# Optimization experiments

Hardware: AMD Instinct MI355X
Metric: run time of the kernel (lower is better)

## Reference

```python
import jax, jax.numpy as jnp
import numpy as np
from jax.scipy.linalg import expm

B, S, D = 8, 2048, 1024          # batch, seq, input_dim
C, CD = 16, 64                   # num_concepts, concept_dim
L = C * CD                       # latent_dim = 1024
ALPHA, BETA = 0.3, 1.0
LN_EPS = 1e-5                    # torch nn.LayerNorm default


def layer_norm(x, g, b):
    m = jnp.mean(x, axis=-1, keepdims=True)
    v = jnp.mean(jnp.square(x - m), axis=-1, keepdims=True)
    return (x - m) * jax.lax.rsqrt(v + LN_EPS) * g + b


def setup_inputs() -> dict:
    key = jax.random.key(0)
    ks = jax.random.split(key, 8)
    sc = 0.02
    return {
        "x": jax.random.normal(ks[0], (B, S, D), jnp.float32),
        # encoder: Linear(D, 2L) + LayerNorm(2L)
        "enc_w": jax.random.normal(ks[1], (2 * L, D), jnp.float32) * sc,
        "enc_b": jnp.zeros((2 * L,), jnp.float32),
        "enc_g": jnp.ones((2 * L,), jnp.float32),
        "enc_bt": jnp.zeros((2 * L,), jnp.float32),
        # DAG weights [C, C] (torch inits zeros; use small random for non-trivial math)
        "dag_w": jax.random.normal(ks[2], (C, C), jnp.float32) * 0.1,
        # per-concept transforms: Linear(CD,CD) -> LN(CD) -> ReLU -> Linear(CD,CD), stacked over C
        "cw1": jax.random.normal(ks[3], (C, CD, CD), jnp.float32) * sc,
        "cb1": jnp.zeros((C, CD), jnp.float32),
        "cg": jnp.ones((C, CD), jnp.float32),
        "cbt": jnp.zeros((C, CD), jnp.float32),
        "cw2": jax.random.normal(ks[4], (C, CD, CD), jnp.float32) * sc,
        "cb2": jnp.zeros((C, CD), jnp.float32),
        # decoder: Linear(L,L) -> LN(L) -> ReLU -> Linear(L,D)
        "dec_w1": jax.random.normal(ks[5], (L, L), jnp.float32) * sc,
        "dec_b1": jnp.zeros((L,), jnp.float32),
        "dec_g": jnp.ones((L,), jnp.float32),
        "dec_bt": jnp.zeros((L,), jnp.float32),
        "dec_w2": jax.random.normal(ks[6], (D, L), jnp.float32) * sc,
        "dec_b2": jnp.zeros((D,), jnp.float32),
    }


def reference(x, enc_w, enc_b, enc_g, enc_bt, dag_w, cw1, cb1, cg, cbt, cw2, cb2,
              dec_w1, dec_b1, dec_g, dec_bt, dec_w2, dec_b2):
    # ---- encode ----
    h = layer_norm(jnp.einsum('bsd,kd->bsk', x, enc_w) + enc_b, enc_g, enc_bt)  # [B,S,2L]
    mu, logvar = jnp.split(h, 2, axis=-1)                                        # [B,S,L] each
    z = mu  # eval-mode reparameterize

    # ---- causal transform ----
    zc = z.reshape(B, S, C, CD)                                   # [B,S,C,CD]
    dag = jnp.tril(jax.nn.softplus(dag_w), k=-1)                  # [C,C]
    z_causal = zc + jnp.einsum('ij,bsjd->bsid', dag, zc)          # [B,S,C,CD]

    # per-concept Linear -> LN -> ReLU -> Linear, batched over concept axis
    t = jnp.einsum('bsce,cde->bscd', z_causal, cw1) + cb1         # [B,S,C,CD]
    t = layer_norm(t, cg, cbt)
    t = jax.nn.relu(t)
    t = jnp.einsum('bsce,cde->bscd', t, cw2) + cb2
    z_t = t.reshape(B, S, L)

    # ---- decode ----
    d = layer_norm(jnp.einsum('bsl,kl->bsk', z_t, dec_w1) + dec_b1, dec_g, dec_bt)
    d = jax.nn.relu(d)
    x_recon = jnp.einsum('bsl,dl->bsd', d, dec_w2) + dec_b2        # [B,S,D]

    # ---- losses ----
    recon_loss = jnp.mean(jnp.square(x_recon - x))
    kl_loss = -0.5 * jnp.mean(1.0 + logvar - jnp.square(mu) - jnp.exp(logvar))
    dag_loss = jnp.sum(jnp.abs(dag)) + jnp.trace(expm(dag))
    total_loss = recon_loss + ALPHA * kl_loss + BETA * dag_loss
    return x_recon, total_loss, kl_loss, recon_loss, dag_loss
```

## Files before the change

kernel.cpp:

```cpp
#include <hip/hip_runtime.h>
#include <stdint.h>


#define NTOK   16384
#define DIM    1024
#define NC     16
#define CD     64
#define NOUT_ELEMS 16777216

typedef float f32x4 __attribute__((ext_vector_type(4)));
typedef __bf16 bf16x8 __attribute__((ext_vector_type(8)));
typedef unsigned short u16x4 __attribute__((ext_vector_type(4)));
typedef unsigned short u16x8 __attribute__((ext_vector_type(8)));

__device__ float g_scal[3];
__device__ float g_part[512];

__device__ __forceinline__ float b2f(uint16_t u) {
  union { uint32_t i; float f; } v; v.i = ((uint32_t)u) << 16; return v.f;
}
__device__ __forceinline__ uint16_t f2b(float f) {
  union { float f; uint32_t i; } v; v.f = f;
  uint32_t x = v.i;
  return (uint16_t)((x + 0x7fffu + ((x >> 16) & 1u)) >> 16);
}

__device__ __forceinline__ void gload_lds16(const uint16_t* g, uint16_t* l) {
  __builtin_amdgcn_global_load_lds(
      (const __attribute__((address_space(1))) void*)g,
      (__attribute__((address_space(3))) void*)l, 16, 0, 0);
}

__device__ __forceinline__ void cvt8(const float* s, uint16_t* d) {
  const f32x4 a = *(const f32x4*)s;
  const f32x4 b = *(const f32x4*)(s + 4);
  u16x8 o;
  o[0]=f2b(a[0]); o[1]=f2b(a[1]); o[2]=f2b(a[2]); o[3]=f2b(a[3]);
  o[4]=f2b(b[0]); o[5]=f2b(b[1]); o[6]=f2b(b[2]); o[7]=f2b(b[3]);
  *(u16x8*)d = o;
}

__global__ __launch_bounds__(256) void cvt_x_kernel(
    const float* __restrict__ src, uint16_t* __restrict__ dst)
{
  const int i = blockIdx.x * 256 + threadIdx.x;
  cvt8(src + (size_t)i * 8, dst + (size_t)i * 8);
}

__global__ __launch_bounds__(256) void cvt_weights_kernel(
    const float* __restrict__ ew, const float* __restrict__ d1,
    const float* __restrict__ d2, const float* __restrict__ c1,
    const float* __restrict__ c2, uint16_t* __restrict__ out)
{
  const int i = blockIdx.x * 256 + threadIdx.x;
  const float* src; uint16_t* dst; int off;
  if (i < 262144)      { src = ew; dst = out;           off = i; }
  else if (i < 393216) { src = d1; dst = out + 2097152; off = i - 262144; }
  else if (i < 524288) { src = d2; dst = out + 3145728; off = i - 393216; }
  else if (i < 532480) { src = c1; dst = out + 4194304; off = i - 524288; }
  else                 { src = c2; dst = out + 4259840; off = i - 532480; }
  cvt8(src + (size_t)off * 8, dst + (size_t)off * 8);
}

template<int BM, int BN, int WM, int WN, typename TC, bool SPLIT, bool RECON>
__global__ __launch_bounds__(256) void gemm_bt_kernel(
    const uint16_t* __restrict__ A, const uint16_t* __restrict__ Wm,
    const float* __restrict__ bias, TC* __restrict__ C0, TC* __restrict__ C1,
    const float* __restrict__ Xref,
    int K, int lda, int ldw, int ldc)
{
  constexpr int BK = 64;
  static_assert(WM * WN == 4, "4 waves");
  constexpr int MI = BM / (WM * 16);
  constexpr int NI = BN / (WN * 16);
  constexpr int AI = (BM * BK * 2) / 4096;
  constexpr int WI = (BN * BK * 2) / 4096;

  __shared__ __align__(16) uint16_t lds[BM * BK + BN * BK];
  uint16_t* As = lds;
  uint16_t* Ws = lds + BM * BK;

  const int tid  = threadIdx.x;
  const int wave = tid >> 6;
  const int lane = tid & 63;
  const int q    = lane >> 4;
  const int r16  = lane & 15;
  const int wm   = wave / WN;
  const int wn   = wave % WN;

  const int bm = blockIdx.x * BM;
  const int bn = blockIdx.y * BN;

  const int sr = tid >> 3;
  const int pc = tid & 7;

  f32x4 acc[MI][NI] = {};

  for (int k0 = 0; k0 < K; k0 += BK) {
#pragma unroll
    for (int i = 0; i < AI; ++i) {
      const int r = i * 32 + sr;
      const int c = pc ^ (r & 7);
      const uint16_t* g = A + (size_t)(bm + r) * lda + k0 + c * 8;
      gload_lds16(g, (uint16_t*)((char*)As + i * 4096 + wave * 1024));
    }
#pragma unroll
    for (int i = 0; i < WI; ++i) {
      const int r = i * 32 + sr;
      const int c = pc ^ (r & 7);
      const uint16_t* g = Wm + (size_t)(bn + r) * ldw + k0 + c * 8;
      gload_lds16(g, (uint16_t*)((char*)Ws + i * 4096 + wave * 1024));
    }
    __syncthreads();

#pragma unroll
    for (int ks = 0; ks < 2; ++ks) {
      bf16x8 af[MI], wf[NI];
#pragma unroll
      for (int mi = 0; mi < MI; ++mi) {
        const int row = wm * (MI * 16) + mi * 16 + r16;
        const int c   = (ks * 4 + q) ^ (row & 7);
        af[mi] = *(const bf16x8*)(As + row * BK + c * 8);
      }
#pragma unroll
      for (int ni = 0; ni < NI; ++ni) {
        const int col = wn * (NI * 16) + ni * 16 + r16;
        const int c   = (ks * 4 + q) ^ (col & 7);
        wf[ni] = *(const bf16x8*)(Ws + col * BK + c * 8);
      }
#pragma unroll
      for (int mi = 0; mi < MI; ++mi)
#pragma unroll
        for (int ni = 0; ni < NI; ++ni)
          acc[mi][ni] = __builtin_amdgcn_mfma_f32_16x16x32_bf16(
              af[mi], wf[ni], acc[mi][ni], 0, 0, 0);
    }
    __syncthreads();
  }

  TC* Cq = C0;
  int cb = bn;
  if constexpr (SPLIT) {
    if (bn >= 1024) { Cq = C1; cb = bn - 1024; }
  }
  float rsum = 0.f;
#pragma unroll
  for (int ni = 0; ni < NI; ++ni) {
    const int loc = wn * (NI * 16) + ni * 16 + r16;
    const float bv = bias[bn + loc];
#pragma unroll
    for (int mi = 0; mi < MI; ++mi) {
      const int rbase = bm + wm * (MI * 16) + mi * 16 + q * 4;
#pragma unroll
      for (int r = 0; r < 4; ++r) {
        const float v = acc[mi][ni][r] + bv;
        if constexpr (sizeof(TC) == 2)
          Cq[(size_t)(rbase + r) * ldc + cb + loc] = f2b(v);
        else
          Cq[(size_t)(rbase + r) * ldc + cb + loc] = v;
        if constexpr (RECON) {
          const float dd = v - Xref[(size_t)(rbase + r) * ldc + cb + loc];
          rsum += dd * dd;
        }
      }
    }
  }
  if constexpr (RECON) {
#pragma unroll
    for (int m = 1; m < 64; m <<= 1) rsum += __shfl_xor(rsum, m);
    __shared__ float redR[4];
    if (lane == 0) redR[wave] = rsum;
    __syncthreads();
    if (tid == 0)
      atomicAdd(&g_part[256 + ((blockIdx.x * 8 + blockIdx.y) & 255)],
                redR[0] + redR[1] + redR[2] + redR[3]);
  }
}

__global__ __launch_bounds__(256) void concept_fused_kernel(
    uint16_t* __restrict__ z, const uint16_t* __restrict__ c1b,
    const uint16_t* __restrict__ c2b, const float* __restrict__ cb1,
    const float* __restrict__ cg, const float* __restrict__ cbt,
    const float* __restrict__ cb2)
{
  __shared__ __align__(16) uint16_t Az[128 * 64];
  __shared__ __align__(16) uint16_t W1s[64 * 64];
  __shared__ __align__(16) uint16_t W2s[64 * 64];

  const int tid  = threadIdx.x;
  const int wave = tid >> 6;
  const int lane = tid & 63;
  const int q    = lane >> 4;
  const int r16  = lane & 15;
  const int c    = blockIdx.y;
  const int m0   = blockIdx.x * 128;

  const int lr = tid >> 3;
  const int pc = tid & 7;

#pragma unroll
  for (int i = 0; i < 4; ++i) {
    const int r = i * 32 + lr;
    const int gc = pc ^ (r & 7);
    gload_lds16(z + (size_t)(m0 + r) * DIM + c * 64 + gc * 8,
                (uint16_t*)((char*)Az + i * 4096 + wave * 1024));
  }
#pragma unroll
  for (int i = 0; i < 2; ++i) {
    const int r = i * 32 + lr;
    const int gc = pc ^ (r & 7);
    gload_lds16(c1b + (size_t)c * 4096 + r * 64 + gc * 8,
                (uint16_t*)((char*)W1s + i * 4096 + wave * 1024));
    gload_lds16(c2b + (size_t)c * 4096 + r * 64 + gc * 8,
                (uint16_t*)((char*)W2s + i * 4096 + wave * 1024));
  }
  __syncthreads();

  f32x4 acc[2][4] = {};
#pragma unroll
  for (int ks = 0; ks < 2; ++ks) {
    bf16x8 af[2], wf[4];
#pragma unroll
    for (int mi = 0; mi < 2; ++mi) {
      const int row = wave * 32 + mi * 16 + r16;
      af[mi] = *(const bf16x8*)(Az + row * 64 + ((ks * 4 + q) ^ (row & 7)) * 8);
    }
#pragma unroll
    for (int ni = 0; ni < 4; ++ni) {
      const int d = ni * 16 + r16;
      wf[ni] = *(const bf16x8*)(W1s + d * 64 + ((ks * 4 + q) ^ (d & 7)) * 8);
    }
#pragma unroll
    for (int mi = 0; mi < 2; ++mi)
#pragma unroll
      for (int ni = 0; ni < 4; ++ni)
        acc[mi][ni] = __builtin_amdgcn_mfma_f32_16x16x32_bf16(
            af[mi], wf[ni], acc[mi][ni], 0, 0, 0);
  }

  float b1v[4], cgv[4], cbv[4], b2v[4];
#pragma unroll
  for (int ni = 0; ni < 4; ++ni) {
    const int cn = ni * 16 + r16;
    b1v[ni] = cb1[c * 64 + cn];
    cgv[ni] = cg[c * 64 + cn];
    cbv[ni] = cbt[c * 64 + cn];
    b2v[ni] = cb2[c * 64 + cn];
  }
#pragma unroll
  for (int mi = 0; mi < 2; ++mi) {
#pragma unroll
    for (int r = 0; r < 4; ++r) {
      float s1 = 0.f, s2 = 0.f;
#pragma unroll
      for (int ni = 0; ni < 4; ++ni) {
        const float v = acc[mi][ni][r] + b1v[ni];
        acc[mi][ni][r] = v;
        s1 += v; s2 += v * v;
      }
#pragma unroll
      for (int m = 1; m < 16; m <<= 1) {
        s1 += __shfl_xor(s1, m);
        s2 += __shfl_xor(s2, m);
      }
      const float mean = s1 * (1.f / 64.f);
      const float var  = s2 * (1.f / 64.f) - mean * mean;
      const float rs   = rsqrtf(var + 1e-5f);
      const int row = wave * 32 + mi * 16 + q * 4 + r;
#pragma unroll
      for (int ni = 0; ni < 4; ++ni) {
        const float y = fmaxf((acc[mi][ni][r] - mean) * rs * cgv[ni] + cbv[ni], 0.f);
        const int cn = ni * 16 + r16;
        Az[row * 64 + (((cn >> 3) ^ (row & 7)) * 8) + (cn & 7)] = f2b(y);
      }
    }
  }
  __syncthreads();

  f32x4 acc2[2][4] = {};
#pragma unroll
  for (int ks = 0; ks < 2; ++ks) {
    bf16x8 af[2], wf[4];
#pragma unroll
    for (int mi = 0; mi < 2; ++mi) {
      const int row = wave * 32 + mi * 16 + r16;
      af[mi] = *(const bf16x8*)(Az + row * 64 + ((ks * 4 + q) ^ (row & 7)) * 8);
    }
#pragma unroll
    for (int ni = 0; ni < 4; ++ni) {
      const int d = ni * 16 + r16;
      wf[ni] = *(const bf16x8*)(W2s + d * 64 + ((ks * 4 + q) ^ (d & 7)) * 8);
    }
#pragma unroll
    for (int mi = 0; mi < 2; ++mi)
#pragma unroll
      for (int ni = 0; ni < 4; ++ni)
        acc2[mi][ni] = __builtin_amdgcn_mfma_f32_16x16x32_bf16(
            af[mi], wf[ni], acc2[mi][ni], 0, 0, 0);
  }

#pragma unroll
  for (int mi = 0; mi < 2; ++mi)
#pragma unroll
    for (int ni = 0; ni < 4; ++ni) {
      const int cn = ni * 16 + r16;
#pragma unroll
      for (int r = 0; r < 4; ++r) {
        const int row = wave * 32 + mi * 16 + q * 4 + r;
        z[(size_t)(m0 + row) * DIM + c * 64 + cn] = f2b(acc2[mi][ni][r] + b2v[ni]);
      }
    }
}

__global__ __launch_bounds__(256) void kl_causal_kernel(
    const uint16_t* __restrict__ lv, uint16_t* __restrict__ mu,
    const float* __restrict__ g, const float* __restrict__ b,
    const float* __restrict__ dag_w)
{
  __shared__ __align__(16) float zsh[1024];
  __shared__ float dg[256];
  __shared__ float red[8];
  __shared__ float red2[4];
  const int tid = threadIdx.x;
  const int tok = blockIdx.x;
  const int e0  = tid * 4;

  {
    const int di = tid >> 4, dj = tid & 15;
    dg[tid] = (dj < di) ? log1pf(expf(dag_w[tid])) : 0.f;
  }

  const uint16_t* lvp = lv + (size_t)tok * 1024;
  uint16_t*       mup = mu + (size_t)tok * 1024;

  const u16x4 m4 = *(const u16x4*)(mup + e0);
  const u16x4 l4 = *(const u16x4*)(lvp + e0);
  float xm[4], xl[4];
  float s1 = 0.f, s2 = 0.f;
#pragma unroll
  for (int k = 0; k < 4; ++k) {
    xm[k] = b2f(m4[k]);
    xl[k] = b2f(l4[k]);
    s1 += xm[k] + xl[k];
    s2 += xm[k] * xm[k] + xl[k] * xl[k];
  }
#pragma unroll
  for (int m = 1; m < 64; m <<= 1) {
    s1 += __shfl_xor(s1, m);
    s2 += __shfl_xor(s2, m);
  }
  const int wave = tid >> 6, lane = tid & 63;
  if (lane == 0) { red[wave] = s1; red[4 + wave] = s2; }
  __syncthreads();
  s1 = red[0] + red[1] + red[2] + red[3];
  s2 = red[4] + red[5] + red[6] + red[7];
  const float mean = s1 * (1.f / 2048.f);
  const float var  = s2 * (1.f / 2048.f) - mean * mean;
  const float rs   = rsqrtf(var + 1e-5f);

  const f32x4 g4m = *(const f32x4*)(g + e0);
  const f32x4 b4m = *(const f32x4*)(b + e0);
  const f32x4 g4l = *(const f32x4*)(g + 1024 + e0);
  const f32x4 b4l = *(const f32x4*)(b + 1024 + e0);
  float kl = 0.f;
  f32x4 z;
#pragma unroll
  for (int k = 0; k < 4; ++k) {
    z[k] = (xm[k] - mean) * rs * g4m[k] + b4m[k];
    const float y = (xl[k] - mean) * rs * g4l[k] + b4l[k];
    kl += 1.f + y - z[k] * z[k] - expf(y);
  }
  *(f32x4*)(zsh + e0) = z;
#pragma unroll
  for (int m = 1; m < 64; m <<= 1) kl += __shfl_xor(kl, m);
  if (lane == 0) red2[wave] = kl;
  __syncthreads();
  if (tid == 0)
    atomicAdd(&g_part[tok & 255], red2[0] + red2[1] + red2[2] + red2[3]);

  const int i  = e0 >> 6;
  const int d0 = e0 & 63;
  f32x4 s = *(const f32x4*)(zsh + e0);
  for (int j = 0; j < i; ++j) {
    const float w = dg[i * 16 + j];
    const f32x4 zj = *(const f32x4*)(zsh + j * 64 + d0);
    s[0] += w * zj[0]; s[1] += w * zj[1]; s[2] += w * zj[2]; s[3] += w * zj[3];
  }
  u16x4 o;
#pragma unroll
  for (int k = 0; k < 4; ++k) o[k] = f2b(s[k]);
  *(u16x4*)(mup + e0) = o;
}

__global__ __launch_bounds__(256) void ln_relu_kernel(
    uint16_t* __restrict__ data, const float* __restrict__ g,
    const float* __restrict__ b)
{
  const int tid = threadIdx.x;
  const int e0  = tid * 4;
  uint16_t* p = data + (size_t)blockIdx.x * 1024;

  const u16x4 v4 = *(const u16x4*)(p + e0);
  float x[4];
  float s1 = 0.f, s2 = 0.f;
#pragma unroll
  for (int k = 0; k < 4; ++k) {
    x[k] = b2f(v4[k]);
    s1 += x[k];
    s2 += x[k] * x[k];
  }
#pragma unroll
  for (int m = 1; m < 64; m <<= 1) {
    s1 += __shfl_xor(s1, m);
    s2 += __shfl_xor(s2, m);
  }
  __shared__ float red[8];
  const int wave = tid >> 6, lane = tid & 63;
  if (lane == 0) { red[wave] = s1; red[4 + wave] = s2; }
  __syncthreads();
  s1 = red[0] + red[1] + red[2] + red[3];
  s2 = red[4] + red[5] + red[6] + red[7];
  const float mean = s1 * (1.f / 1024.f);
  const float var  = s2 * (1.f / 1024.f) - mean * mean;
  const float rs   = rsqrtf(var + 1e-5f);

  const f32x4 g4 = *(const f32x4*)(g + e0);
  const f32x4 b4 = *(const f32x4*)(b + e0);
  u16x4 o;
#pragma unroll
  for (int k = 0; k < 4; ++k) {
    const float y = (x[k] - mean) * rs * g4[k] + b4[k];
    o[k] = f2b(fmaxf(y, 0.f));
  }
  *(u16x4*)(p + e0) = o;
}

__global__ __launch_bounds__(256) void dag_init_kernel(
    const float* __restrict__ dag_w)
{
  const int t = threadIdx.x;
  g_part[t] = 0.f;
  g_part[256 + t] = 0.f;
  const int i = t >> 4, j = t & 15;
  const float v = (j < i) ? log1pf(expf(dag_w[t])) : 0.f;
  float s = v;
#pragma unroll
  for (int m = 1; m < 64; m <<= 1) s += __shfl_xor(s, m);
  __shared__ float red[4];
  const int wave = t >> 6, lane = t & 63;
  if (lane == 0) red[wave] = s;
  __syncthreads();
  if (t == 0)
    g_scal[2] = red[0] + red[1] + red[2] + red[3] + 16.f;
}

__global__ __launch_bounds__(256) void finalize_kernel(float* __restrict__ out_tail)
{
  const int tid = threadIdx.x;
  float kl = g_part[tid];
  float rc = g_part[256 + tid];
#pragma unroll
  for (int m = 1; m < 64; m <<= 1) {
    kl += __shfl_xor(kl, m);
    rc += __shfl_xor(rc, m);
  }
  __shared__ float red[8];
  const int wave = tid >> 6, lane = tid & 63;
  if (lane == 0) { red[wave] = kl; red[4 + wave] = rc; }
  __syncthreads();
  if (tid == 0) {
    const float kls = red[0] + red[1] + red[2] + red[3];
    const float rcs = red[4] + red[5] + red[6] + red[7];
    const float kl_l   = -0.5f * kls * (1.f / (16384.f * 1024.f));
    const float recon  = rcs * (1.f / 16777216.f);
    const float dagl   = g_scal[2];
    out_tail[0] = recon + 0.3f * kl_l + 1.0f * dagl;
    out_tail[1] = kl_l;
    out_tail[2] = recon;
    out_tail[3] = dagl;
  }
}

extern "C" void kernel_launch(void* const* d_in, const int* in_sizes, int n_in,
                              void* d_out, int out_size, void* d_ws, size_t ws_size,
                              hipStream_t stream) {
  const float* x      = (const float*)d_in[0];
  const float* enc_w  = (const float*)d_in[1];
  const float* enc_b  = (const float*)d_in[2];
  const float* enc_g  = (const float*)d_in[3];
  const float* enc_bt = (const float*)d_in[4];
  const float* dag_w  = (const float*)d_in[5];
  const float* cw1    = (const float*)d_in[6];
  const float* cb1    = (const float*)d_in[7];
  const float* cg     = (const float*)d_in[8];
  const float* cbt    = (const float*)d_in[9];
  const float* cw2    = (const float*)d_in[10];
  const float* cb2    = (const float*)d_in[11];
  const float* dec_w1 = (const float*)d_in[12];
  const float* dec_b1 = (const float*)d_in[13];
  const float* dec_g  = (const float*)d_in[14];
  const float* dec_bt = (const float*)d_in[15];
  const float* dec_w2 = (const float*)d_in[16];
  const float* dec_b2 = (const float*)d_in[17];

  uint16_t* S    = (uint16_t*)d_ws;
  uint16_t* Wbf  = (uint16_t*)((char*)d_ws + (size_t)NTOK * DIM * 2);
  uint16_t* ewb  = Wbf;
  uint16_t* d1b  = Wbf + 2097152;
  uint16_t* d2b  = Wbf + 3145728;
  uint16_t* c1b  = Wbf + 4194304;
  uint16_t* c2b  = Wbf + 4259840;

  uint16_t* Obf  = (uint16_t*)d_out;
  uint16_t* xbf  = Obf + (size_t)NOUT_ELEMS;
  float*    O    = (float*)d_out;

  dag_init_kernel<<<1, 256, 0, stream>>>(dag_w);

  cvt_x_kernel<<<NOUT_ELEMS / 8 / 256, 256, 0, stream>>>(x, xbf);
  cvt_weights_kernel<<<2112, 256, 0, stream>>>(enc_w, dec_w1, dec_w2, cw1, cw2, Wbf);

  gemm_bt_kernel<128, 128, 2, 2, uint16_t, true, false>
      <<<dim3(128, 16, 1), 256, 0, stream>>>(
      xbf, ewb, enc_b, Obf, S, nullptr, DIM, DIM, DIM, DIM);

  kl_causal_kernel<<<NTOK, 256, 0, stream>>>(S, Obf, enc_g, enc_bt, dag_w);

  concept_fused_kernel<<<dim3(128, 16, 1), 256, 0, stream>>>(
      Obf, c1b, c2b, cb1, cg, cbt, cb2);

  gemm_bt_kernel<128, 128, 2, 2, uint16_t, false, false>
      <<<dim3(128, 8, 1), 256, 0, stream>>>(
      Obf, d1b, dec_b1, S, S, nullptr, DIM, DIM, DIM, DIM);

  ln_relu_kernel<<<NTOK, 256, 0, stream>>>(S, dec_g, dec_bt);

  gemm_bt_kernel<128, 128, 2, 2, float, false, true>
      <<<dim3(128, 8, 1), 256, 0, stream>>>(
      S, d2b, dec_b2, O, O, x, DIM, DIM, DIM, DIM);

  finalize_kernel<<<1, 256, 0, stream>>>(O + (size_t)NOUT_ELEMS);
}
```

Measured before the change: 424.6 us.

## Replace GEMM with 256x256 tile, 8-wave double-buffered pipelined kernel

Replaces the 128x128 single-buffered GEMM with a 256x256 tile kernel using 8 waves, double-buffered LDS staging, and global loads for the next tiles issued in the middle of the MFMA loop. It also remaps workgroup IDs with an XCD-aware swizzle and raises MFMA priority with setprio. The aim is to hide global-load latency and cut redundant tile traffic. In exchange it uses 128KB of LDS per block, so occupancy is lower, and with fewer blocks the launch may leave some CUs underfilled.

```diff
diff --git a/kernel.cpp b/kernel.cpp
--- a/kernel.cpp
+++ b/kernel.cpp
@@ -62,80 +62,120 @@
   cvt8(src + (size_t)off * 8, dst + (size_t)off * 8);
 }
 
-template<int BM, int BN, int WM, int WN, typename TC, bool SPLIT, bool RECON>
-__global__ __launch_bounds__(256) void gemm_bt_kernel(
+__device__ __forceinline__ void stage_half(
+    const uint16_t* __restrict__ G, uint16_t* L, int h, int lda,
+    int sr, int pc, int wave)
+{
+#pragma unroll
+  for (int i = 0; i < 2; ++i) {
+    const int r = h * 128 + i * 64 + sr;
+    gload_lds16(G + (size_t)r * lda + (size_t)((pc ^ (sr & 7)) * 8),
+                (uint16_t*)((char*)L + h * 16384 + i * 8192 + wave * 1024));
+  }
+}
+
+template<typename TC, bool SPLIT, bool RECON>
+__global__ __launch_bounds__(512, 2) void gemm256_kernel(
     const uint16_t* __restrict__ A, const uint16_t* __restrict__ Wm,
     const float* __restrict__ bias, TC* __restrict__ C0, TC* __restrict__ C1,
     const float* __restrict__ Xref,
     int K, int lda, int ldw, int ldc)
 {
-  constexpr int BK = 64;
-  static_assert(WM * WN == 4, "4 waves");
-  constexpr int MI = BM / (WM * 16);
-  constexpr int NI = BN / (WN * 16);
-  constexpr int AI = (BM * BK * 2) / 4096;
-  constexpr int WI = (BN * BK * 2) / 4096;
-
-  __shared__ __align__(16) uint16_t lds[BM * BK + BN * BK];
-  uint16_t* As = lds;
-  uint16_t* Ws = lds + BM * BK;
+  __shared__ __align__(16) uint16_t lds[65536];
 
   const int tid  = threadIdx.x;
   const int wave = tid >> 6;
   const int lane = tid & 63;
   const int q    = lane >> 4;
   const int r16  = lane & 15;
-  const int wm   = wave / WN;
-  const int wn   = wave % WN;
-
-  const int bm = blockIdx.x * BM;
-  const int bn = blockIdx.y * BN;
-
-  const int sr = tid >> 3;
-  const int pc = tid & 7;
-
-  f32x4 acc[MI][NI] = {};
-
-  for (int k0 = 0; k0 < K; k0 += BK) {
-#pragma unroll
-    for (int i = 0; i < AI; ++i) {
-      const int r = i * 32 + sr;
-      const int c = pc ^ (r & 7);
-      const uint16_t* g = A + (size_t)(bm + r) * lda + k0 + c * 8;
-      gload_lds16(g, (uint16_t*)((char*)As + i * 4096 + wave * 1024));
-    }
-#pragma unroll
-    for (int i = 0; i < WI; ++i) {
-      const int r = i * 32 + sr;
-      const int c = pc ^ (r & 7);
-      const uint16_t* g = Wm + (size_t)(bn + r) * ldw + k0 + c * 8;
-      gload_lds16(g, (uint16_t*)((char*)Ws + i * 4096 + wave * 1024));
-    }
-    __syncthreads();
-
-#pragma unroll
-    for (int ks = 0; ks < 2; ++ks) {
-      bf16x8 af[MI], wf[NI];
-#pragma unroll
-      for (int mi = 0; mi < MI; ++mi) {
-        const int row = wm * (MI * 16) + mi * 16 + r16;
-        const int c   = (ks * 4 + q) ^ (row & 7);
-        af[mi] = *(const bf16x8*)(As + row * BK + c * 8);
-      }
-#pragma unroll
-      for (int ni = 0; ni < NI; ++ni) {
-        const int col = wn * (NI * 16) + ni * 16 + r16;
-        const int c   = (ks * 4 + q) ^ (col & 7);
-        wf[ni] = *(const bf16x8*)(Ws + col * BK + c * 8);
-      }
-#pragma unroll
-      for (int mi = 0; mi < MI; ++mi)
-#pragma unroll
-        for (int ni = 0; ni < NI; ++ni)
-          acc[mi][ni] = __builtin_amdgcn_mfma_f32_16x16x32_bf16(
-              af[mi], wf[ni], acc[mi][ni], 0, 0, 0);
-    }
-    __syncthreads();
+  const int wm   = wave >> 2;
+  const int wn   = wave & 3;
+  const int sr   = tid >> 3;
+  const int pc   = tid & 7;
+
+  const int gx  = gridDim.x;
+  const int nwg = gx * gridDim.y;
+  int o = blockIdx.y * gx + blockIdx.x;
+  o = (o & 7) * (nwg >> 3) + (o >> 3);
+  const int bm = (o % gx) * 256;
+  const int bn = (o / gx) * 256;
+
+  const uint16_t* Ab = A  + (size_t)bm * lda;
+  const uint16_t* Wb = Wm + (size_t)bn * ldw;
+
+  const int T = K >> 6;
+
+  stage_half(Ab,      lds,                 0, lda, sr, pc, wave);
+  stage_half(Ab,      lds,                 1, lda, sr, pc, wave);
+  stage_half(Wb,      lds + 16384,         0, ldw, sr, pc, wave);
+  stage_half(Wb,      lds + 16384,         1, ldw, sr, pc, wave);
+  if (T > 1) {
+    stage_half(Wb + 64, lds + 32768 + 16384, 0, ldw, sr, pc, wave);
+    stage_half(Wb + 64, lds + 32768 + 16384, 1, ldw, sr, pc, wave);
+    asm volatile("s_waitcnt vmcnt(4)" ::: "memory");
+  } else {
+    asm volatile("s_waitcnt vmcnt(0)" ::: "memory");
+  }
+  __builtin_amdgcn_s_barrier();
+
+  f32x4 acc[8][4] = {};
+  const int cxa = r16 & 7;
+  const int c0  = (q ^ cxa) * 8;
+  const int c1  = ((4 + q) ^ cxa) * 8;
+
+  for (int t = 0; t < T; ++t) {
+    uint16_t* As  = lds + (t & 1) * 32768;
+    uint16_t* Bs  = As + 16384;
+    uint16_t* Asn = lds + ((t & 1) ^ 1) * 32768;
+
+    const uint16_t* a_rd = As + (wm * 128 + r16) * 64;
+    const uint16_t* b_rd = Bs + (wn * 64  + r16) * 64;
+
+    bf16x8 bfr[4][2];
+
+#pragma unroll
+    for (int p = 0; p < 4; ++p) {
+      bf16x8 af[2][2];
+#pragma unroll
+      for (int mi2 = 0; mi2 < 2; ++mi2) {
+        af[mi2][0] = *(const bf16x8*)(a_rd + (p * 2 + mi2) * 1024 + c0);
+        af[mi2][1] = *(const bf16x8*)(a_rd + (p * 2 + mi2) * 1024 + c1);
+      }
+      if (p == 0) {
+#pragma unroll
+        for (int ni = 0; ni < 4; ++ni) {
+          bfr[ni][0] = *(const bf16x8*)(b_rd + ni * 1024 + c0);
+          bfr[ni][1] = *(const bf16x8*)(b_rd + ni * 1024 + c1);
+        }
+        if (t + 1 < T) {
+          stage_half(Ab + (size_t)(t + 1) * 64, Asn, 0, lda, sr, pc, wave);
+          stage_half(Ab + (size_t)(t + 1) * 64, Asn, 1, lda, sr, pc, wave);
+        }
+      } else if (p == 1) {
+        if (t + 2 < T)
+          stage_half(Wb + (size_t)(t + 2) * 64, Bs, 0, ldw, sr, pc, wave);
+      } else if (p == 2) {
+        if (t + 2 < T)
+          stage_half(Wb + (size_t)(t + 2) * 64, Bs, 1, ldw, sr, pc, wave);
+      }
+
+      __builtin_amdgcn_s_barrier();
+      __builtin_amdgcn_s_setprio(1);
+#pragma unroll
+      for (int ks = 0; ks < 2; ++ks)
+#pragma unroll
+        for (int mi2 = 0; mi2 < 2; ++mi2)
+#pragma unroll
+          for (int ni = 0; ni < 4; ++ni)
+            acc[p * 2 + mi2][ni] = __builtin_amdgcn_mfma_f32_16x16x32_bf16(
+                af[mi2][ks], bfr[ni][ks], acc[p * 2 + mi2][ni], 0, 0, 0);
+      __builtin_amdgcn_s_setprio(0);
+      if (p == 3) {
+        if (t + 2 < T)      asm volatile("s_waitcnt vmcnt(4)" ::: "memory");
+        else if (t + 1 < T) asm volatile("s_waitcnt vmcnt(0)" ::: "memory");
+      }
+      __builtin_amdgcn_s_barrier();
+    }
   }
 
   TC* Cq = C0;
@@ -145,12 +185,12 @@
   }
   float rsum = 0.f;
 #pragma unroll
-  for (int ni = 0; ni < NI; ++ni) {
-    const int loc = wn * (NI * 16) + ni * 16 + r16;
+  for (int ni = 0; ni < 4; ++ni) {
+    const int loc = wn * 64 + ni * 16 + r16;
     const float bv = bias[bn + loc];
 #pragma unroll
-    for (int mi = 0; mi < MI; ++mi) {
-      const int rbase = bm + wm * (MI * 16) + mi * 16 + q * 4;
+    for (int mi = 0; mi < 8; ++mi) {
+      const int rbase = bm + wm * 128 + mi * 16 + q * 4;
 #pragma unroll
       for (int r = 0; r < 4; ++r) {
         const float v = acc[mi][ni][r] + bv;
@@ -168,12 +208,15 @@
   if constexpr (RECON) {
 #pragma unroll
     for (int m = 1; m < 64; m <<= 1) rsum += __shfl_xor(rsum, m);
-    __shared__ float redR[4];
+    __shared__ float redR[8];
     if (lane == 0) redR[wave] = rsum;
     __syncthreads();
-    if (tid == 0)
-      atomicAdd(&g_part[256 + ((blockIdx.x * 8 + blockIdx.y) & 255)],
-                redR[0] + redR[1] + redR[2] + redR[3]);
+    if (tid == 0) {
+      float s = 0.f;
+#pragma unroll
+      for (int w2 = 0; w2 < 8; ++w2) s += redR[w2];
+      atomicAdd(&g_part[256 + (o & 255)], s);
+    }
   }
 }
 
@@ -520,8 +563,8 @@
   cvt_x_kernel<<<NOUT_ELEMS / 8 / 256, 256, 0, stream>>>(x, xbf);
   cvt_weights_kernel<<<2112, 256, 0, stream>>>(enc_w, dec_w1, dec_w2, cw1, cw2, Wbf);
 
-  gemm_bt_kernel<128, 128, 2, 2, uint16_t, true, false>
-      <<<dim3(128, 16, 1), 256, 0, stream>>>(
+  gemm256_kernel<uint16_t, true, false>
+      <<<dim3(64, 8, 1), 512, 0, stream>>>(
       xbf, ewb, enc_b, Obf, S, nullptr, DIM, DIM, DIM, DIM);
 
   kl_causal_kernel<<<NTOK, 256, 0, stream>>>(S, Obf, enc_g, enc_bt, dag_w);
@@ -529,14 +572,14 @@
   concept_fused_kernel<<<dim3(128, 16, 1), 256, 0, stream>>>(
       Obf, c1b, c2b, cb1, cg, cbt, cb2);
 
-  gemm_bt_kernel<128, 128, 2, 2, uint16_t, false, false>
-      <<<dim3(128, 8, 1), 256, 0, stream>>>(
+  gemm256_kernel<uint16_t, false, false>
+      <<<dim3(64, 4, 1), 512, 0, stream>>>(
       Obf, d1b, dec_b1, S, S, nullptr, DIM, DIM, DIM, DIM);
 
   ln_relu_kernel<<<NTOK, 256, 0, stream>>>(S, dec_g, dec_bt);
 
-  gemm_bt_kernel<128, 128, 2, 2, float, false, true>
-      <<<dim3(128, 8, 1), 256, 0, stream>>>(
+  gemm256_kernel<float, false, true>
+      <<<dim3(64, 4, 1), 512, 0, stream>>>(
       S, d2b, dec_b2, O, O, x, DIM, DIM, DIM, DIM);
 
   finalize_kernel<<<1, 256, 0, stream>>>(O + (size_t)NOUT_ELEMS);
```

Result: no change. 418.8 us (-1.3%).
